# Kernel optimization log

Measured on AMD Instinct MI355X. Metric: run time of the kernel, lower is better.

Reference implementation:

```python
import jax, jax.numpy as jnp
import numpy as np

BATCH, IN, OUT = 4096, 4096, 4096

def setup_inputs() -> dict:
    key = jax.random.key(0)
    kx, kw, kb = jax.random.split(key, 3)
    x = jax.random.normal(kx, (BATCH, IN), dtype=jnp.float32)
    weights = jax.random.normal(kw, (OUT, IN), dtype=jnp.float32)
    beta = jax.random.normal(kb, (1,), dtype=jnp.float32)
    return {"x": x, "weights": weights, "beta": beta}

def reference(x, weights, beta):
    # original: sum over input dim of broadcast multiply == x @ W^T
    row_sum = jnp.einsum('bi,oi->bo', x, weights)  # [batch, output]
    return jax.nn.relu(1.0 - beta + row_sum)
```

## Files before the change

kernel.cpp:

```cpp
#include <hip/hip_runtime.h>
#include <hip/hip_bf16.h>
#include <cstdint>
#include <cstddef>

#define MDIM 4096
#define NDIM 4096
#define KDIM 4096

#define BM 256
#define BN 256
#define BK 64
#define NT (KDIM / BK)

typedef __bf16 bf16_t;
typedef bf16_t bf16x8 __attribute__((ext_vector_type(8)));
typedef float f32x4 __attribute__((ext_vector_type(4)));

#define GLDS16(gsrc, ldst)                                                   \
    __builtin_amdgcn_global_load_lds(                                        \
        (__attribute__((address_space(1))) void*)(gsrc),                     \
        (__attribute__((address_space(3))) void*)(ldst), 16, 0, 0)

#define BAR()   __builtin_amdgcn_s_barrier()
#define VM4()   asm volatile("s_waitcnt vmcnt(4)" ::: "memory")
#define VM0()   asm volatile("s_waitcnt vmcnt(0)" ::: "memory")
#define PRIO1() __builtin_amdgcn_s_setprio(1)
#define PRIO0() __builtin_amdgcn_s_setprio(0)

__device__ __forceinline__ int swz(int q) { return q ^ (((q >> 7) & 7) << 4); }

__global__ void cvt_f32_to_bf16(const float* __restrict__ src,
                                bf16_t* __restrict__ dst, int n) {
    int idx = (blockIdx.x * blockDim.x + threadIdx.x) * 8;
    int stride = gridDim.x * blockDim.x * 8;
    for (int i = idx; i < n; i += stride) {
        const float4* s = reinterpret_cast<const float4*>(src + i);
        float4 a = s[0];
        float4 b = s[1];
        bf16x8 o;
        o[0] = (bf16_t)a.x; o[1] = (bf16_t)a.y;
        o[2] = (bf16_t)a.z; o[3] = (bf16_t)a.w;
        o[4] = (bf16_t)b.x; o[5] = (bf16_t)b.y;
        o[6] = (bf16_t)b.z; o[7] = (bf16_t)b.w;
        *reinterpret_cast<bf16x8*>(dst + i) = o;
    }
}


#define LOAD_A_HALF(MH, BUF) do {                                            \
  _Pragma("unroll") for (int mi = 0; mi < 4; ++mi)                           \
  _Pragma("unroll") for (int ko = 0; ko < 2; ++ko)                           \
    av[mi][ko] = *(const bf16x8*)(ldsb + ((BUF) << 16) + a_off[(MH)*4 + mi][ko]); \
} while (0)

#define LOAD_B_PAIR(NH, BUF) do {                                            \
  _Pragma("unroll") for (int ni = 0; ni < 2; ++ni)                           \
  _Pragma("unroll") for (int ko = 0; ko < 2; ++ko)                           \
    bv[(NH)*2 + ni][ko] = *(const bf16x8*)(ldsb + ((BUF) << 16) + b_off[(NH)*2 + ni][ko]); \
} while (0)

#define MFMA_QUAD(MH, NH) do {                                               \
  _Pragma("unroll") for (int mi = 0; mi < 4; ++mi)                           \
  _Pragma("unroll") for (int ni = 0; ni < 2; ++ni)                           \
  _Pragma("unroll") for (int ko = 0; ko < 2; ++ko)                           \
    acc[(MH)*4 + mi][(NH)*2 + ni] = __builtin_amdgcn_mfma_f32_16x16x32_bf16( \
        av[mi][ko], bv[(NH)*2 + ni][ko], acc[(MH)*4 + mi][(NH)*2 + ni], 0, 0, 0); \
} while (0)

#define TILE(T, BUF) do {                                                    \
                                                                     \
    LOAD_A_HALF(0, BUF); LOAD_B_PAIR(0, BUF);                                \
    if ((T) + 1 < NT) stA((T) + 1, (BUF) ^ 1, 1);                            \
    PRIO1(); MFMA_QUAD(0, 0); PRIO0();                                       \
    BAR();                                                                   \
                                                                     \
    LOAD_B_PAIR(1, BUF);                                                     \
    if ((T) + 1 < NT) stB((T) + 1, (BUF) ^ 1, 1);                            \
    PRIO1(); MFMA_QUAD(0, 1); PRIO0();                                       \
    BAR();                                                                   \
                                                                     \
    LOAD_A_HALF(1, BUF);                                                     \
    if ((T) + 2 < NT) stB((T) + 2, (BUF), 0);                                \
    PRIO1(); MFMA_QUAD(1, 0); PRIO0();                                       \
    BAR();                                                                   \
                                                                     \
    if ((T) + 2 < NT) stA((T) + 2, (BUF), 0);                                \
    PRIO1(); MFMA_QUAD(1, 1); PRIO0();                                       \
    if ((T) < NT - 2) { VM4(); } else { VM0(); }                             \
    BAR();                                                                   \
} while (0)

__global__ __launch_bounds__(512, 2) void gemm256(const bf16_t* __restrict__ A,
                                                  const bf16_t* __restrict__ B,
                                                  const float* __restrict__ beta,
                                                  float* __restrict__ out) {
    extern __shared__ char ldsb[];

    const int tid    = threadIdx.x;
    const int wid    = tid >> 6;
    const int lane   = tid & 63;
    const int warp_m = wid >> 2;
    const int warp_n = wid & 3;
    const int lrow   = lane & 15;
    const int kgrp   = lane >> 4;

    const int bid  = blockIdx.x;
    const int sbid = (bid & 7) * 32 + (bid >> 3);
    const int brow = (sbid >> 4) * BM;
    const int bcol = (sbid & 15) * BN;

    const int p0 = tid * 16, p1 = (tid + 512) * 16;
    const int q0 = swz(p0), q1 = swz(p1);
    const int rh0 = q0 >> 7, ce0 = (q0 & 127) >> 1;
    const int rh1 = q1 >> 7, ce1 = (q1 & 127) >> 1;

    const bf16_t* gA = A + (size_t)brow * KDIM;
    const bf16_t* gB = B + (size_t)bcol * KDIM;

    int off[2][2];
#pragma unroll
    for (int h = 0; h < 2; ++h) {
        off[h][0] = (h * 128 + rh0) * KDIM + ce0;
        off[h][1] = (h * 128 + rh1) * KDIM + ce1;
    }

    auto stA = [&](int t, int buf, int h) {
        const bf16_t* g = gA + t * BK;
        char* d = ldsb + (buf << 16) + (h << 14);
        GLDS16(g + off[h][0], d + p0);
        GLDS16(g + off[h][1], d + p1);
    };
    auto stB = [&](int t, int buf, int h) {
        const bf16_t* g = gB + t * BK;
        char* d = ldsb + (buf << 16) + ((2 + h) << 14);
        GLDS16(g + off[h][0], d + p0);
        GLDS16(g + off[h][1], d + p1);
    };

    int a_off[8][2];
#pragma unroll
    for (int mi = 0; mi < 8; ++mi)
#pragma unroll
        for (int ko = 0; ko < 2; ++ko)
            a_off[mi][ko] = (warp_m << 14) +
                swz((mi * 16 + lrow) * 128 + (ko * 32 + kgrp * 8) * 2);
    int b_off[4][2];
#pragma unroll
    for (int ni = 0; ni < 4; ++ni)
#pragma unroll
        for (int ko = 0; ko < 2; ++ko)
            b_off[ni][ko] = ((2 + (warp_n >> 1)) << 14) +
                swz(((warp_n & 1) * 64 + ni * 16 + lrow) * 128 + (ko * 32 + kgrp * 8) * 2);

    f32x4 acc[8][4];
#pragma unroll
    for (int i = 0; i < 8; ++i)
#pragma unroll
        for (int j = 0; j < 4; ++j)
            acc[i][j] = (f32x4){0.f, 0.f, 0.f, 0.f};

    bf16x8 av[4][2];
    bf16x8 bv[4][2];

    stA(0, 0, 0); stA(0, 0, 1); stB(0, 0, 0); stB(0, 0, 1);
    stB(1, 1, 0); stA(1, 1, 0);
    VM4();
    BAR();

    for (int t = 0; t < NT; t += 2) {
        TILE(t, 0);
        TILE(t + 1, 1);
    }

    const float bias = 1.0f - beta[0];
    float* outp = out + (size_t)(brow + warp_m * 128) * NDIM + bcol + warp_n * 64;
#pragma unroll
    for (int mi = 0; mi < 8; ++mi)
#pragma unroll
        for (int ni = 0; ni < 4; ++ni)
#pragma unroll
            for (int j = 0; j < 4; ++j) {
                const int r = mi * 16 + kgrp * 4 + j;
                const int c = ni * 16 + lrow;
                outp[(size_t)r * NDIM + c] = fmaxf(acc[mi][ni][j] + bias, 0.0f);
            }
}

__global__ void gemm_f32_fallback(const float* __restrict__ A,
                                  const float* __restrict__ B,
                                  const float* __restrict__ beta,
                                  float* __restrict__ out) {
    __shared__ float sA[16][17];
    __shared__ float sB[16][17];
    const int tx = threadIdx.x, ty = threadIdx.y;
    const int m = blockIdx.y * 16 + ty;
    const int n = blockIdx.x * 16 + tx;
    float acc = 0.f;
    for (int k0 = 0; k0 < KDIM; k0 += 16) {
        sA[ty][tx] = A[(size_t)m * KDIM + k0 + tx];
        sB[ty][tx] = B[(size_t)(blockIdx.x * 16 + ty) * KDIM + k0 + tx];
        __syncthreads();
#pragma unroll
        for (int k = 0; k < 16; ++k)
            acc += sA[ty][k] * sB[tx][k];
        __syncthreads();
    }
    float v = acc + 1.0f - beta[0];
    out[(size_t)m * NDIM + n] = fmaxf(v, 0.f);
}

extern "C" void kernel_launch(void* const* d_in, const int* in_sizes, int n_in,
                              void* d_out, int out_size, void* d_ws, size_t ws_size,
                              hipStream_t stream) {
    const float* x    = (const float*)d_in[0];
    const float* w    = (const float*)d_in[1];
    const float* beta = (const float*)d_in[2];
    float* out        = (float*)d_out;

    const size_t nelem = (size_t)MDIM * (size_t)KDIM;
    const size_t need  = 2 * nelem * sizeof(bf16_t);

    if (ws_size >= need) {
        bf16_t* xb = (bf16_t*)d_ws;
        bf16_t* wb = xb + nelem;
        hipFuncSetAttribute((const void*)gemm256,
                            hipFuncAttributeMaxDynamicSharedMemorySize, 131072);
        cvt_f32_to_bf16<<<2048, 256, 0, stream>>>(x, xb, (int)nelem);
        cvt_f32_to_bf16<<<2048, 256, 0, stream>>>(w, wb, (int)nelem);
        gemm256<<<256, 512, 131072, stream>>>(xb, wb, beta, out);
    } else {
        dim3 grid(NDIM / 16, MDIM / 16);
        gemm_f32_fallback<<<grid, dim3(16, 16), 0, stream>>>(x, w, beta, out);
    }
}
```

Baseline: 174.7 us.

## Switch GEMM inner loop to 32x32x16 MFMA with extra barrier and LDS waits

Replaces the 16x16x32 bf16 MFMA tiling with 32x32x16 MFMA instructions, reorganising per-warp fragments into 4x2 32x32 accumulators and recomputing LDS read offsets and output indexing. Larger MFMA tiles halve the fragment reads per flop and use the higher-throughput instruction shape. It also inserts an extra barrier and an lgkmcnt(0) wait before each MFMA quad, which serialises LDS reads against compute and may reduce overlap.

```diff
diff --git a/kernel.cpp b/kernel.cpp
--- a/kernel.cpp
+++ b/kernel.cpp
@@ -14,7 +14,7 @@
 
 typedef __bf16 bf16_t;
 typedef bf16_t bf16x8 __attribute__((ext_vector_type(8)));
-typedef float f32x4 __attribute__((ext_vector_type(4)));
+typedef float f32x16 __attribute__((ext_vector_type(16)));
 
 #define GLDS16(gsrc, ldst)                                                   \
     __builtin_amdgcn_global_load_lds(                                        \
@@ -22,6 +22,7 @@
         (__attribute__((address_space(3))) void*)(ldst), 16, 0, 0)
 
 #define BAR()   __builtin_amdgcn_s_barrier()
+#define LGKM0() asm volatile("s_waitcnt lgkmcnt(0)" ::: "memory")
 #define VM4()   asm volatile("s_waitcnt vmcnt(4)" ::: "memory")
 #define VM0()   asm volatile("s_waitcnt vmcnt(0)" ::: "memory")
 #define PRIO1() __builtin_amdgcn_s_setprio(1)
@@ -48,43 +49,47 @@
 
 
 #define LOAD_A_HALF(MH, BUF) do {                                            \
-  _Pragma("unroll") for (int mi = 0; mi < 4; ++mi)                           \
-  _Pragma("unroll") for (int ko = 0; ko < 2; ++ko)                           \
-    av[mi][ko] = *(const bf16x8*)(ldsb + ((BUF) << 16) + a_off[(MH)*4 + mi][ko]); \
+  _Pragma("unroll") for (int u = 0; u < 2; ++u)                              \
+  _Pragma("unroll") for (int ks = 0; ks < 4; ++ks)                           \
+    av[u][ks] = *(const bf16x8*)(ldsb + ((BUF) << 16) + aB[ks] +             \
+                                 ((MH)*2 + u) * 4096);                       \
 } while (0)
 
 #define LOAD_B_PAIR(NH, BUF) do {                                            \
-  _Pragma("unroll") for (int ni = 0; ni < 2; ++ni)                           \
-  _Pragma("unroll") for (int ko = 0; ko < 2; ++ko)                           \
-    bv[(NH)*2 + ni][ko] = *(const bf16x8*)(ldsb + ((BUF) << 16) + b_off[(NH)*2 + ni][ko]); \
+  _Pragma("unroll") for (int ks = 0; ks < 4; ++ks)                           \
+    bv[NH][ks] = *(const bf16x8*)(ldsb + ((BUF) << 16) + bB[ks] +            \
+                                  (NH) * 4096);                              \
 } while (0)
 
 #define MFMA_QUAD(MH, NH) do {                                               \
-  _Pragma("unroll") for (int mi = 0; mi < 4; ++mi)                           \
-  _Pragma("unroll") for (int ni = 0; ni < 2; ++ni)                           \
-  _Pragma("unroll") for (int ko = 0; ko < 2; ++ko)                           \
-    acc[(MH)*4 + mi][(NH)*2 + ni] = __builtin_amdgcn_mfma_f32_16x16x32_bf16( \
-        av[mi][ko], bv[(NH)*2 + ni][ko], acc[(MH)*4 + mi][(NH)*2 + ni], 0, 0, 0); \
+  _Pragma("unroll") for (int u = 0; u < 2; ++u)                              \
+  _Pragma("unroll") for (int ks = 0; ks < 4; ++ks)                           \
+    acc[(MH)*2 + u][NH] = __builtin_amdgcn_mfma_f32_32x32x16_bf16(           \
+        av[u][ks], bv[NH][ks], acc[(MH)*2 + u][NH], 0, 0, 0);                \
 } while (0)
 
 #define TILE(T, BUF) do {                                                    \
                                                                      \
     LOAD_A_HALF(0, BUF); LOAD_B_PAIR(0, BUF);                                \
     if ((T) + 1 < NT) stA((T) + 1, (BUF) ^ 1, 1);                            \
+    BAR(); LGKM0();                                                          \
     PRIO1(); MFMA_QUAD(0, 0); PRIO0();                                       \
     BAR();                                                                   \
                                                                      \
     LOAD_B_PAIR(1, BUF);                                                     \
     if ((T) + 1 < NT) stB((T) + 1, (BUF) ^ 1, 1);                            \
+    BAR(); LGKM0();                                                          \
     PRIO1(); MFMA_QUAD(0, 1); PRIO0();                                       \
     BAR();                                                                   \
                                                                      \
     LOAD_A_HALF(1, BUF);                                                     \
     if ((T) + 2 < NT) stB((T) + 2, (BUF), 0);                                \
+    BAR(); LGKM0();                                                          \
     PRIO1(); MFMA_QUAD(1, 0); PRIO0();                                       \
     BAR();                                                                   \
                                                                      \
     if ((T) + 2 < NT) stA((T) + 2, (BUF), 0);                                \
+    BAR(); LGKM0();                                                          \
     PRIO1(); MFMA_QUAD(1, 1); PRIO0();                                       \
     if ((T) < NT - 2) { VM4(); } else { VM0(); }                             \
     BAR();                                                                   \
@@ -101,8 +106,8 @@
     const int lane   = tid & 63;
     const int warp_m = wid >> 2;
     const int warp_n = wid & 3;
-    const int lrow   = lane & 15;
-    const int kgrp   = lane >> 4;
+    const int l31    = lane & 31;
+    const int khalf  = lane >> 5;
 
     const int bid  = blockIdx.x;
     const int sbid = (bid & 7) * 32 + (bid >> 3);
@@ -137,30 +142,24 @@
         GLDS16(g + off[h][1], d + p1);
     };
 
-    int a_off[8][2];
-#pragma unroll
-    for (int mi = 0; mi < 8; ++mi)
-#pragma unroll
-        for (int ko = 0; ko < 2; ++ko)
-            a_off[mi][ko] = (warp_m << 14) +
-                swz((mi * 16 + lrow) * 128 + (ko * 32 + kgrp * 8) * 2);
-    int b_off[4][2];
-#pragma unroll
-    for (int ni = 0; ni < 4; ++ni)
-#pragma unroll
-        for (int ko = 0; ko < 2; ++ko)
-            b_off[ni][ko] = ((2 + (warp_n >> 1)) << 14) +
-                swz(((warp_n & 1) * 64 + ni * 16 + lrow) * 128 + (ko * 32 + kgrp * 8) * 2);
-
-    f32x4 acc[8][4];
-#pragma unroll
-    for (int i = 0; i < 8; ++i)
-#pragma unroll
-        for (int j = 0; j < 4; ++j)
-            acc[i][j] = (f32x4){0.f, 0.f, 0.f, 0.f};
-
-    bf16x8 av[4][2];
-    bf16x8 bv[4][2];
+    const int kx = (l31 & 7) << 4;
+    int aB[4], bB[4];
+#pragma unroll
+    for (int ks = 0; ks < 4; ++ks) {
+        const int kb = (ks * 32 + khalf * 16) ^ kx;
+        aB[ks] = (warp_m << 14) + l31 * 128 + kb;
+        bB[ks] = ((2 + (warp_n >> 1)) << 14) + ((warp_n & 1) * 64 + l31) * 128 + kb;
+    }
+
+    f32x16 acc[4][2];
+#pragma unroll
+    for (int i = 0; i < 4; ++i)
+#pragma unroll
+        for (int j = 0; j < 2; ++j)
+            acc[i][j] = (f32x16)(0.f);
+
+    bf16x8 av[2][4];
+    bf16x8 bv[2][4];
 
     stA(0, 0, 0); stA(0, 0, 1); stB(0, 0, 0); stB(0, 0, 1);
     stB(1, 1, 0); stA(1, 1, 0);
@@ -175,14 +174,14 @@
     const float bias = 1.0f - beta[0];
     float* outp = out + (size_t)(brow + warp_m * 128) * NDIM + bcol + warp_n * 64;
 #pragma unroll
-    for (int mi = 0; mi < 8; ++mi)
-#pragma unroll
-        for (int ni = 0; ni < 4; ++ni)
-#pragma unroll
-            for (int j = 0; j < 4; ++j) {
-                const int r = mi * 16 + kgrp * 4 + j;
-                const int c = ni * 16 + lrow;
-                outp[(size_t)r * NDIM + c] = fmaxf(acc[mi][ni][j] + bias, 0.0f);
+    for (int mi = 0; mi < 4; ++mi)
+#pragma unroll
+        for (int ni = 0; ni < 2; ++ni)
+#pragma unroll
+            for (int reg = 0; reg < 16; ++reg) {
+                const int r = mi * 32 + (reg & 3) + 8 * (reg >> 2) + 4 * khalf;
+                const int c = ni * 32 + l31;
+                outp[(size_t)r * NDIM + c] = fmaxf(acc[mi][ni][reg] + bias, 0.0f);
             }
 }
 
```

Measured after the change: 166.6 us. -4.6%, faster.
